# Kernel tuning notes

Measured on AMD Instinct MI355X. Metric: run time of the kernel, lower is better.

## Reference

```python
import jax, jax.numpy as jnp
import numpy as np

REGION_MAX = 116
DEFAULT_REGION_ID = 0


def setup_inputs() -> dict:
    key = jax.random.key(0)
    k1, k2, k3, k4 = jax.random.split(key, 4)
    B, N = 16, 4096
    D, H, W = 182, 218, 182
    embed_dim = 768
    # patch centers in MRI voxel space; range slightly exceeds the atlas so
    # some points land out-of-bounds and exercise the default-region path.
    patch_centers_voxels = jax.random.uniform(k1, (B, N, 3), dtype=jnp.float32) * 230.0 - 20.0
    # use identity-like affines (typical co-registered case)
    mri_affine = jnp.eye(4, dtype=jnp.float32)
    aal_affine = jnp.eye(4, dtype=jnp.float32)
    # atlas volume with integer region labels stored as float (nib get_fdata)
    aal_data = jax.random.randint(k3, (D, H, W), 0, REGION_MAX + 1).astype(jnp.float32)
    embed_table = jax.random.normal(k4, (REGION_MAX + 1, embed_dim), dtype=jnp.float32)
    return {
        "patch_centers_voxels": patch_centers_voxels,
        "mri_affine": mri_affine,
        "aal_affine": aal_affine,
        "aal_data": aal_data,
        "embed_table": embed_table,
    }


def reference(patch_centers_voxels, mri_affine, aal_affine, aal_data, embed_table):
    B, N, _ = patch_centers_voxels.shape
    D, H, W = aal_data.shape
    # homogeneous voxel coords -> world coords -> atlas voxel coords
    ones = jnp.ones((B, N, 1), dtype=patch_centers_voxels.dtype)
    voxel_homo = jnp.concatenate([patch_centers_voxels, ones], axis=-1)  # [B,N,4]
    world = jnp.einsum('ij,bnj->bni', mri_affine, voxel_homo)
    inv_aal = jnp.linalg.inv(aal_affine)
    aal_vox = jnp.einsum('ij,bnj->bni', inv_aal, world)[..., :3]  # [B,N,3]
    idx = jnp.round(aal_vox).astype(jnp.int32)  # [B,N,3]
    x, y, z = idx[..., 0], idx[..., 1], idx[..., 2]
    in_bounds = (
        (x >= 0) & (x < D) & (y >= 0) & (y < H) & (z >= 0) & (z < W)
    )
    cx = jnp.clip(x, 0, D - 1)
    cy = jnp.clip(y, 0, H - 1)
    cz = jnp.clip(z, 0, W - 1)
    region = aal_data[cx, cy, cz].astype(jnp.int32)  # [B,N]
    valid = in_bounds & (region >= 0) & (region <= REGION_MAX)
    region_ids = jnp.where(valid, region, DEFAULT_REGION_ID)
    return embed_table[region_ids]  # [B,N,embed_dim]
```

## Files before the change

kernel.cpp:

```cpp
#include <hip/hip_runtime.h>
#include <math.h>

#define REGION_MAX 116
#define EMB 768
#define EMB4 192
#define DIM_D 182
#define DIM_H 218
#define DIM_W 182
#define PPB 32
#define BLOCK 256

typedef float v4f __attribute__((ext_vector_type(4)));

__global__ __launch_bounds__(BLOCK) void fused_embed_kernel(
    const float* __restrict__ centers,
    const float* __restrict__ mri,
    const float* __restrict__ aal,
    const float* __restrict__ vol,
    const float* __restrict__ table,
    float* __restrict__ out,
    int P) {
    __shared__ float M[12];
    __shared__ int rids[PPB];

    if (threadIdx.x == 0) {
        float a[4][8];
        for (int i = 0; i < 4; ++i)
            for (int j = 0; j < 4; ++j) {
                a[i][j]     = aal[i * 4 + j];
                a[i][j + 4] = (i == j) ? 1.0f : 0.0f;
            }
        for (int c = 0; c < 4; ++c) {
            int piv = c;
            float best = fabsf(a[c][c]);
            for (int r = c + 1; r < 4; ++r) {
                float v = fabsf(a[r][c]);
                if (v > best) { best = v; piv = r; }
            }
            if (piv != c)
                for (int j = 0; j < 8; ++j) {
                    float t = a[c][j]; a[c][j] = a[piv][j]; a[piv][j] = t;
                }
            float inv = 1.0f / a[c][c];
            for (int j = 0; j < 8; ++j) a[c][j] *= inv;
            for (int r = 0; r < 4; ++r) {
                if (r == c) continue;
                float f = a[r][c];
                for (int j = 0; j < 8; ++j) a[r][j] -= f * a[c][j];
            }
        }
        for (int i = 0; i < 3; ++i)
            for (int j = 0; j < 4; ++j) {
                float s = 0.0f;
                for (int k = 0; k < 4; ++k) s += a[i][4 + k] * mri[k * 4 + j];
                M[i * 4 + j] = s;
            }
    }
    __syncthreads();

    const int base = blockIdx.x * PPB;

    if (threadIdx.x < PPB) {
        const int p = base + threadIdx.x;
        int r = 0;
        if (p < P) {
            float px = centers[p * 3 + 0];
            float py = centers[p * 3 + 1];
            float pz = centers[p * 3 + 2];

            float fx = M[0] * px + M[1] * py + M[2]  * pz + M[3];
            float fy = M[4] * px + M[5] * py + M[6]  * pz + M[7];
            float fz = M[8] * px + M[9] * py + M[10] * pz + M[11];

            int x = (int)rintf(fx);
            int y = (int)rintf(fy);
            int z = (int)rintf(fz);

            bool inb = (x >= 0) & (x < DIM_D) & (y >= 0) & (y < DIM_H) &
                       (z >= 0) & (z < DIM_W);
            int cx = min(max(x, 0), DIM_D - 1);
            int cy = min(max(y, 0), DIM_H - 1);
            int cz = min(max(z, 0), DIM_W - 1);

            int region = (int)vol[((size_t)cx * DIM_H + cy) * DIM_W + cz];
            r = (inb && region >= 0 && region <= REGION_MAX) ? region : 0;
        }
        rids[threadIdx.x] = r;
    }
    __syncthreads();

    const int npts = min(PPB, P - base);
    const v4f* __restrict__ tab4 = (const v4f*)table;
    v4f* __restrict__ out4 = (v4f*)out + (long)base * EMB4;

    if (npts == PPB) {
        #pragma unroll 4
        for (unsigned j = threadIdx.x; j < (unsigned)(PPB * EMB4); j += BLOCK) {
            unsigned p = j / (unsigned)EMB4;
            unsigned c = j - p * (unsigned)EMB4;
            v4f v = tab4[(unsigned)rids[p] * EMB4 + c];
            __builtin_nontemporal_store(v, out4 + j);
        }
    } else {
        for (unsigned j = threadIdx.x; j < (unsigned)(npts * EMB4); j += BLOCK) {
            unsigned p = j / (unsigned)EMB4;
            unsigned c = j - p * (unsigned)EMB4;
            v4f v = tab4[(unsigned)rids[p] * EMB4 + c];
            __builtin_nontemporal_store(v, out4 + j);
        }
    }
}

extern "C" void kernel_launch(void* const* d_in, const int* in_sizes, int n_in,
                              void* d_out, int out_size, void* d_ws, size_t ws_size,
                              hipStream_t stream) {
    const float* centers = (const float*)d_in[0];
    const float* mri     = (const float*)d_in[1];
    const float* aal     = (const float*)d_in[2];
    const float* vol     = (const float*)d_in[3];
    const float* table   = (const float*)d_in[4];
    float* out = (float*)d_out;

    int P = in_sizes[0] / 3;
    int blocks = (P + PPB - 1) / PPB;
    fused_embed_kernel<<<blocks, BLOCK, 0, stream>>>(
        centers, mri, aal, vol, table, out, P);
}
```

Baseline: 232.1 us.

## Bucket points by region and scatter each embedding row from shared memory

Replaces the single fused gather kernel with four kernels. They zero per-region counters, bucket point indices by region with atomics, prefix-sum the buckets into 32-point work units, and have each block load one table row into shared memory and scatter it to that unit's output rows. The goal is to avoid repeated global gathers of table rows. In exchange it adds three extra launches, an atomic-heavy bucketing pass, and scattered non-contiguous output writes. It also needs a large workspace (117*P ints) and falls back to the old kernel when the workspace is too small.

```diff
diff --git a/kernel.cpp b/kernel.cpp
--- a/kernel.cpp
+++ b/kernel.cpp
@@ -2,6 +2,7 @@
 #include <math.h>
 
 #define REGION_MAX 116
+#define NREG 117
 #define EMB 768
 #define EMB4 192
 #define DIM_D 182
@@ -10,104 +11,159 @@
 #define PPB 32
 #define BLOCK 256
 
+#define NUNITS_OFF 128
+#define UNITS_OFF  256
+#define LIST_OFF   8192
+
 typedef float v4f __attribute__((ext_vector_type(4)));
 
+__device__ __forceinline__ void compute_M(const float* __restrict__ mri,
+                                          const float* __restrict__ aal,
+                                          float* M ) {
+    float a[4][8];
+    for (int i = 0; i < 4; ++i)
+        for (int j = 0; j < 4; ++j) {
+            a[i][j]     = aal[i * 4 + j];
+            a[i][j + 4] = (i == j) ? 1.0f : 0.0f;
+        }
+    for (int c = 0; c < 4; ++c) {
+        int piv = c;
+        float best = fabsf(a[c][c]);
+        for (int r = c + 1; r < 4; ++r) {
+            float v = fabsf(a[r][c]);
+            if (v > best) { best = v; piv = r; }
+        }
+        if (piv != c)
+            for (int j = 0; j < 8; ++j) {
+                float t = a[c][j]; a[c][j] = a[piv][j]; a[piv][j] = t;
+            }
+        float inv = 1.0f / a[c][c];
+        for (int j = 0; j < 8; ++j) a[c][j] *= inv;
+        for (int r = 0; r < 4; ++r) {
+            if (r == c) continue;
+            float f = a[r][c];
+            for (int j = 0; j < 8; ++j) a[r][j] -= f * a[c][j];
+        }
+    }
+    for (int i = 0; i < 3; ++i)
+        for (int j = 0; j < 4; ++j) {
+            float s = 0.0f;
+            for (int k = 0; k < 4; ++k) s += a[i][4 + k] * mri[k * 4 + j];
+            M[i * 4 + j] = s;
+        }
+}
+
+__device__ __forceinline__ int region_of(const float* __restrict__ centers,
+                                         const float* __restrict__ vol,
+                                         const float* M, int p) {
+    float px = centers[p * 3 + 0];
+    float py = centers[p * 3 + 1];
+    float pz = centers[p * 3 + 2];
+    float fx = M[0] * px + M[1] * py + M[2]  * pz + M[3];
+    float fy = M[4] * px + M[5] * py + M[6]  * pz + M[7];
+    float fz = M[8] * px + M[9] * py + M[10] * pz + M[11];
+    int x = (int)rintf(fx);
+    int y = (int)rintf(fy);
+    int z = (int)rintf(fz);
+    bool inb = (x >= 0) & (x < DIM_D) & (y >= 0) & (y < DIM_H) &
+               (z >= 0) & (z < DIM_W);
+    int cx = min(max(x, 0), DIM_D - 1);
+    int cy = min(max(y, 0), DIM_H - 1);
+    int cz = min(max(z, 0), DIM_W - 1);
+    int region = (int)vol[((size_t)cx * DIM_H + cy) * DIM_W + cz];
+    return (inb && region >= 0 && region <= REGION_MAX) ? region : 0;
+}
+
+__global__ void k0_zero(int* __restrict__ ws) {
+    if (threadIdx.x < NREG) ws[threadIdx.x] = 0;
+}
+
+__global__ __launch_bounds__(BLOCK) void k1_region(
+    const float* __restrict__ centers, const float* __restrict__ mri,
+    const float* __restrict__ aal, const float* __restrict__ vol,
+    int* __restrict__ ws, int P) {
+    __shared__ float M[12];
+    if (threadIdx.x == 0) compute_M(mri, aal, M);
+    __syncthreads();
+    int p = blockIdx.x * blockDim.x + threadIdx.x;
+    if (p >= P) return;
+    int r = region_of(centers, vol, M, p);
+    int slot = atomicAdd(&ws[r], 1);
+    ws[LIST_OFF + r * P + slot] = p;
+}
+
+__global__ void k2_units(int* __restrict__ ws) {
+    __shared__ int sc[128];
+    int t = threadIdx.x;
+    int c = 0;
+    if (t < NREG) c = (ws[t] + PPB - 1) / PPB;
+    sc[t] = c;
+    __syncthreads();
+    for (int off = 1; off < 128; off <<= 1) {
+        int add = (t >= off) ? sc[t - off] : 0;
+        __syncthreads();
+        sc[t] += add;
+        __syncthreads();
+    }
+    int start = sc[t] - c;
+    if (t < NREG)
+        for (int k = 0; k < c; ++k)
+            ws[UNITS_OFF + start + k] = (k << 8) | t;
+    if (t == 127) ws[NUNITS_OFF] = sc[127];
+}
+
+__global__ __launch_bounds__(BLOCK) void k3_scatter(
+    const int* __restrict__ ws, const float* __restrict__ table,
+    float* __restrict__ out, int P) {
+    __shared__ v4f row[EMB4];
+    __shared__ int pid[PPB];
+    const int nunits = ws[NUNITS_OFF];
+    const v4f* __restrict__ tab4 = (const v4f*)table;
+    for (int u = blockIdx.x; u < nunits; u += gridDim.x) {
+        int e = ws[UNITS_OFF + u];
+        int r = e & 255;
+        int c = e >> 8;
+        int base = c * PPB;
+        int n = min(PPB, ws[r] - base);
+        const int* __restrict__ lst = ws + LIST_OFF + r * P + base;
+        __syncthreads();
+        if (threadIdx.x < EMB4) row[threadIdx.x] = tab4[r * EMB4 + threadIdx.x];
+        if (threadIdx.x < n)    pid[threadIdx.x] = lst[threadIdx.x];
+        __syncthreads();
+        unsigned tot = (unsigned)n * EMB4;
+        #pragma unroll 4
+        for (unsigned j = threadIdx.x; j < tot; j += BLOCK) {
+            unsigned pl = j / EMB4;
+            unsigned c4 = j - pl * EMB4;
+            v4f v = row[c4];
+            __builtin_nontemporal_store(
+                v, (v4f*)out + (unsigned)pid[pl] * EMB4 + c4);
+        }
+    }
+}
+
 __global__ __launch_bounds__(BLOCK) void fused_embed_kernel(
-    const float* __restrict__ centers,
-    const float* __restrict__ mri,
-    const float* __restrict__ aal,
-    const float* __restrict__ vol,
-    const float* __restrict__ table,
-    float* __restrict__ out,
-    int P) {
+    const float* __restrict__ centers, const float* __restrict__ mri,
+    const float* __restrict__ aal, const float* __restrict__ vol,
+    const float* __restrict__ table, float* __restrict__ out, int P) {
     __shared__ float M[12];
     __shared__ int rids[PPB];
-
-    if (threadIdx.x == 0) {
-        float a[4][8];
-        for (int i = 0; i < 4; ++i)
-            for (int j = 0; j < 4; ++j) {
-                a[i][j]     = aal[i * 4 + j];
-                a[i][j + 4] = (i == j) ? 1.0f : 0.0f;
-            }
-        for (int c = 0; c < 4; ++c) {
-            int piv = c;
-            float best = fabsf(a[c][c]);
-            for (int r = c + 1; r < 4; ++r) {
-                float v = fabsf(a[r][c]);
-                if (v > best) { best = v; piv = r; }
-            }
-            if (piv != c)
-                for (int j = 0; j < 8; ++j) {
-                    float t = a[c][j]; a[c][j] = a[piv][j]; a[piv][j] = t;
-                }
-            float inv = 1.0f / a[c][c];
-            for (int j = 0; j < 8; ++j) a[c][j] *= inv;
-            for (int r = 0; r < 4; ++r) {
-                if (r == c) continue;
-                float f = a[r][c];
-                for (int j = 0; j < 8; ++j) a[r][j] -= f * a[c][j];
-            }
-        }
-        for (int i = 0; i < 3; ++i)
-            for (int j = 0; j < 4; ++j) {
-                float s = 0.0f;
-                for (int k = 0; k < 4; ++k) s += a[i][4 + k] * mri[k * 4 + j];
-                M[i * 4 + j] = s;
-            }
+    if (threadIdx.x == 0) compute_M(mri, aal, M);
+    __syncthreads();
+    const int base = blockIdx.x * PPB;
+    if (threadIdx.x < PPB) {
+        const int p = base + threadIdx.x;
+        rids[threadIdx.x] = (p < P) ? region_of(centers, vol, M, p) : 0;
     }
     __syncthreads();
-
-    const int base = blockIdx.x * PPB;
-
-    if (threadIdx.x < PPB) {
-        const int p = base + threadIdx.x;
-        int r = 0;
-        if (p < P) {
-            float px = centers[p * 3 + 0];
-            float py = centers[p * 3 + 1];
-            float pz = centers[p * 3 + 2];
-
-            float fx = M[0] * px + M[1] * py + M[2]  * pz + M[3];
-            float fy = M[4] * px + M[5] * py + M[6]  * pz + M[7];
-            float fz = M[8] * px + M[9] * py + M[10] * pz + M[11];
-
-            int x = (int)rintf(fx);
-            int y = (int)rintf(fy);
-            int z = (int)rintf(fz);
-
-            bool inb = (x >= 0) & (x < DIM_D) & (y >= 0) & (y < DIM_H) &
-                       (z >= 0) & (z < DIM_W);
-            int cx = min(max(x, 0), DIM_D - 1);
-            int cy = min(max(y, 0), DIM_H - 1);
-            int cz = min(max(z, 0), DIM_W - 1);
-
-            int region = (int)vol[((size_t)cx * DIM_H + cy) * DIM_W + cz];
-            r = (inb && region >= 0 && region <= REGION_MAX) ? region : 0;
-        }
-        rids[threadIdx.x] = r;
-    }
-    __syncthreads();
-
     const int npts = min(PPB, P - base);
     const v4f* __restrict__ tab4 = (const v4f*)table;
     v4f* __restrict__ out4 = (v4f*)out + (long)base * EMB4;
-
-    if (npts == PPB) {
-        #pragma unroll 4
-        for (unsigned j = threadIdx.x; j < (unsigned)(PPB * EMB4); j += BLOCK) {
-            unsigned p = j / (unsigned)EMB4;
-            unsigned c = j - p * (unsigned)EMB4;
-            v4f v = tab4[(unsigned)rids[p] * EMB4 + c];
-            __builtin_nontemporal_store(v, out4 + j);
-        }
-    } else {
-        for (unsigned j = threadIdx.x; j < (unsigned)(npts * EMB4); j += BLOCK) {
-            unsigned p = j / (unsigned)EMB4;
-            unsigned c = j - p * (unsigned)EMB4;
-            v4f v = tab4[(unsigned)rids[p] * EMB4 + c];
-            __builtin_nontemporal_store(v, out4 + j);
-        }
+    for (unsigned j = threadIdx.x; j < (unsigned)(npts * EMB4); j += BLOCK) {
+        unsigned p = j / (unsigned)EMB4;
+        unsigned c = j - p * (unsigned)EMB4;
+        v4f v = tab4[(unsigned)rids[p] * (unsigned)EMB4 + c];
+        __builtin_nontemporal_store(v, out4 + j);
     }
 }
 
@@ -120,9 +176,21 @@
     const float* vol     = (const float*)d_in[3];
     const float* table   = (const float*)d_in[4];
     float* out = (float*)d_out;
+    int*   ws  = (int*)d_ws;
 
     int P = in_sizes[0] / 3;
-    int blocks = (P + PPB - 1) / PPB;
-    fused_embed_kernel<<<blocks, BLOCK, 0, stream>>>(
-        centers, mri, aal, vol, table, out, P);
+    size_t need = ((size_t)LIST_OFF + (size_t)NREG * (size_t)P) * sizeof(int);
+
+    if (ws_size >= need) {
+        int blocks1 = (P + BLOCK - 1) / BLOCK;
+        int blocks3 = 2048;
+        k0_zero<<<1, 128, 0, stream>>>(ws);
+        k1_region<<<blocks1, BLOCK, 0, stream>>>(centers, mri, aal, vol, ws, P);
+        k2_units<<<1, 128, 0, stream>>>(ws);
+        k3_scatter<<<blocks3, BLOCK, 0, stream>>>(ws, table, out, P);
+    } else {
+        int blocks = (P + PPB - 1) / PPB;
+        fused_embed_kernel<<<blocks, BLOCK, 0, stream>>>(
+            centers, mri, aal, vol, table, out, P);
+    }
 }
```

Result: slower. 586.8 us (+152.9%).
